# Kernel tuning notes

Measured on AMD Instinct MI355X. Metric: run time of the kernel, lower is better.

Reference implementation:

```python
import jax, jax.numpy as jnp
import numpy as np

# Representation: lvals=[0,1] -> nreps NL=2, dim DIM=1+3=4; mult=8; kqv conv out_mult=3*mult
N, K, EDGE_DIM, HID = 10000, 16, 32, 64
MULT, NL, DIM = 8, 2, 4
OUT_MULT = 3 * MULT
E = N * K
NHEADS = 4
HEAD_DIM = MULT * DIM // NHEADS  # 8


def setup_inputs() -> dict:
    key = jax.random.key(0)
    ks = jax.random.split(key, 9)
    out_flat = NL * NL * MULT * OUT_MULT  # 768
    return {
        "basis1": jax.random.normal(ks[0], (E, DIM, NL), jnp.float32),
        "basis2": jax.random.normal(ks[1], (E, NL, DIM), jnp.float32),
        "edge_feats": jax.random.normal(ks[2], (E, EDGE_DIM), jnp.float32),
        "f": jax.random.normal(ks[3], (N, MULT, DIM), jnp.float32),
        "W1": jax.random.normal(ks[4], (HID, EDGE_DIM), jnp.float32) / np.sqrt(EDGE_DIM).astype(np.float32),
        "b1": jnp.zeros((HID,), jnp.float32),
        "W2": jax.random.normal(ks[5], (out_flat, HID), jnp.float32) / np.sqrt(HID).astype(np.float32),
        "b2": jnp.zeros((out_flat,), jnp.float32),
        "neighbor_idx": jax.random.randint(ks[6], (N, K), 0, N, dtype=jnp.int32),
    }


def reference(basis1, basis2, edge_feats, f, W1, b1, W2, b2, neighbor_idx):
    src = neighbor_idx.reshape(-1)  # (E,) source node per edge
    # RadialWeight: 2-layer MLP edge_feats -> per-edge TP weights (E, NL*OUT_MULT, NL*MULT)
    h = jax.nn.relu(edge_feats @ W1.T + b1)
    rw = (h @ W2.T + b2).reshape(E, NL * OUT_MULT, NL * MULT)
    # EquivariantConvolution: gather + small batched matmuls
    f_src = f[src]  # (E, MULT, DIM)
    tmp = jnp.einsum('emd,edl->eml', f_src, basis1).reshape(E, NL * MULT, 1)
    tmp = (rw @ tmp).reshape(E, OUT_MULT, NL)
    kqv = jnp.einsum('eml,eld->emd', tmp, basis2)  # (E, 3*MULT, DIM)
    # split fused k/q/v along multiplicity (repr_h.rep2.mult = 3*mult)
    k_, q_, v_ = jnp.split(kqv.reshape(N, K, OUT_MULT, DIM), 3, axis=2)  # each (N,K,MULT,DIM)
    k_ = k_.reshape(N, K, NHEADS, HEAD_DIM)
    v_ = v_.reshape(N, K, NHEADS, HEAD_DIM)
    q_node = q_.reshape(N, K, NHEADS, HEAD_DIM).mean(axis=1)  # per-node query (N,H,hd)
    scale = HEAD_DIM ** -0.5
    scores = jnp.einsum('nhd,nkhd->nhk', q_node, k_) * scale  # (N,H,K)
    w = jax.nn.softmax(scores, axis=-1)
    out = jnp.einsum('nhk,nkhd->nhd', w, v_)  # (N,H,hd)
    return out.reshape(N, MULT, DIM)
```

## Files before the change

kernel.cpp:

```cpp
#include <hip/hip_runtime.h>
#include <hip/hip_bf16.h>
#include <math.h>

#define N_NODES 10000
#define KNBR    16
#define EDGEF   32
#define HID     64
#define MULT    8
#define NL      2
#define DIM     4
#define OUT_MULT 24
#define NHEADS  4
#define HEAD_DIM 8
#define E_TOT   (N_NODES*KNBR)

#define EPB 128
#define TPB 256
#define NODES_PB 8
#define NSLICE 33

typedef float    f32x4 __attribute__((ext_vector_type(4)));
typedef _Float16 f16x8 __attribute__((ext_vector_type(8)));

#define BF1_HALVES (4*64*8)
#define BF2_HALVES (3*NSLICE*64*8)
#define WS_HALVES  (BF1_HALVES + BF2_HALVES)

__global__ __launch_bounds__(256)
void esa_prep(const float* __restrict__ W1, const float* __restrict__ W2,
              const float* __restrict__ b2, _Float16* __restrict__ wsh)
{
    int i = blockIdx.x * 256 + threadIdx.x;
    if (i >= WS_HALVES) return;
    float v;
    if (i < BF1_HALVES) {
        int j = i & 7, lane = (i >> 3) & 63, t = i >> 9;
        int k = ((lane >> 4) << 3) + j;
        int n = (t << 4) + (lane & 15);
        v = W1[n * EDGEF + k];
    } else {
        int i2 = i - BF1_HALVES;
        int j = i2 & 7, lane = (i2 >> 3) & 63;
        int st = i2 >> 9;
        int s = st % NSLICE, t = st / NSLICE;
        int k = (s << 5) + ((lane >> 4) << 3) + j;
        int n = (t << 4) + (lane & 15);
        if (k < 1024)      v = W2[(n * 16 + (k >> 6)) * HID + (k & 63)];
        else if (k < 1040) v = b2[n * 16 + (k - 1024)];
        else               v = 0.f;
    }
    wsh[i] = (_Float16)v;
}

__global__ __launch_bounds__(TPB, 4)
void esa_main(const float* __restrict__ basis1, const float* __restrict__ basis2,
              const float* __restrict__ edge_feats, const float* __restrict__ f,
              const float* __restrict__ b1, const int* __restrict__ nbr,
              const _Float16* __restrict__ wsh, float* __restrict__ out)
{
    __shared__ __align__(16) unsigned char smem[32768];
    _Float16* hls = (_Float16*)smem;
    _Float16* tpl = (_Float16*)(smem + 18432);
    float*    t2  = (float*)smem;
    float*    b2l = (float*)(smem + 26624);

    const int tid  = threadIdx.x;
    const int eb   = blockIdx.x * EPB;
    const int lane = tid & 63;
    const int w    = tid >> 6;
    const int lo   = lane & 15, hi = lane >> 4;

    {
        int el = tid >> 1, hf = tid & 1;
        int e  = eb + el;
        int src = nbr[e];
        const float4* b1p = (const float4*)(basis1 + (size_t)e * 8);
        float4 u0 = b1p[0], u1 = b1p[1];
        float bl0[4] = {u0.x, u0.z, u1.x, u1.z};
        float bl1[4] = {u0.y, u0.w, u1.y, u1.w};
        const float4* fp = (const float4*)(f + (size_t)src * 32 + hf * 16);
        _Float16 tpv[8];
        #pragma unroll
        for (int mm = 0; mm < 4; ++mm) {
            float4 fv = fp[mm];
            float a0 = fv.x*bl0[0] + fv.y*bl0[1] + fv.z*bl0[2] + fv.w*bl0[3];
            float a1 = fv.x*bl1[0] + fv.y*bl1[1] + fv.z*bl1[2] + fv.w*bl1[3];
            tpv[mm*2+0] = (_Float16)a0;
            tpv[mm*2+1] = (_Float16)a1;
        }
        *(f16x8*)(tpl + el*16 + hf*8) = *(f16x8*)tpv;
        float4 b2v = ((const float4*)(basis2 + (size_t)e * 8))[hf];
        *((float4*)(b2l + el*12) + hf) = b2v;
    }

    {
        float b1v[4];
        #pragma unroll
        for (int t = 0; t < 4; ++t) b1v[t] = b1[t*16 + lo];
        f16x8 afr[2];
        #pragma unroll
        for (int mt = 0; mt < 2; ++mt) {
            size_t eg = (size_t)(eb + w*32 + mt*16 + lo);
            const float4* p = (const float4*)(edge_feats + eg*32 + hi*8);
            float4 x0 = p[0], x1 = p[1];
            f16x8 a;
            a[0]=(_Float16)x0.x; a[1]=(_Float16)x0.y; a[2]=(_Float16)x0.z; a[3]=(_Float16)x0.w;
            a[4]=(_Float16)x1.x; a[5]=(_Float16)x1.y; a[6]=(_Float16)x1.z; a[7]=(_Float16)x1.w;
            afr[mt] = a;
        }
        #pragma unroll
        for (int t = 0; t < 4; ++t) {
            f16x8 bfr = *(const f16x8*)(wsh + ((size_t)(t*64 + lane)) * 8);
            #pragma unroll
            for (int mt = 0; mt < 2; ++mt) {
                f32x4 acc = {0.f, 0.f, 0.f, 0.f};
                acc = __builtin_amdgcn_mfma_f32_16x16x32_f16(afr[mt], bfr, acc, 0, 0, 0);
                #pragma unroll
                for (int r = 0; r < 4; ++r) {
                    float hv = acc[r] + b1v[t];
                    hv = hv > 0.f ? hv : 0.f;
                    int el = w*32 + mt*16 + hi*4 + r;
                    hls[el*72 + t*16 + lo] = (_Float16)hv;
                }
            }
        }
    }
    __syncthreads();

    f32x4 acc[2][3];
    #pragma unroll
    for (int mt = 0; mt < 2; ++mt)
        #pragma unroll
        for (int t = 0; t < 3; ++t)
            acc[mt][t] = (f32x4){0.f, 0.f, 0.f, 0.f};

    {
        const _Float16* Bf2 = wsh + BF1_HALVES;
        const int e0 = w*32 + lo;
        const int e1 = e0 + 16;
        const _Float16* hp0 = hls + e0*72 + hi*8;
        const _Float16* hp1 = hls + e1*72 + hi*8;
        f16x8 tp0a = *(const f16x8*)(tpl + e0*16);
        f16x8 tp0b = *(const f16x8*)(tpl + e0*16 + 8);
        f16x8 tp1a = *(const f16x8*)(tpl + e1*16);
        f16x8 tp1b = *(const f16x8*)(tpl + e1*16 + 8);

        #pragma unroll 2
        for (int s = 0; s < 32; ++s) {
            const int c  = s >> 1;
            const int sh = s & 1;
            _Float16 t0 = tpl[e0*16 + c];
            _Float16 t1 = tpl[e1*16 + c];
            f16x8 ts0 = {t0,t0,t0,t0,t0,t0,t0,t0};
            f16x8 ts1 = {t1,t1,t1,t1,t1,t1,t1,t1};
            f16x8 h0 = *(const f16x8*)(hp0 + sh*32);
            f16x8 h1 = *(const f16x8*)(hp1 + sh*32);
            f16x8 a0 = h0 * ts0;
            f16x8 a1 = h1 * ts1;
            #pragma unroll
            for (int t = 0; t < 3; ++t) {
                f16x8 bfr = *(const f16x8*)(Bf2 + ((size_t)((t*NSLICE + s)*64 + lane)) * 8);
                acc[0][t] = __builtin_amdgcn_mfma_f32_16x16x32_f16(a0, bfr, acc[0][t], 0, 0, 0);
                acc[1][t] = __builtin_amdgcn_mfma_f32_16x16x32_f16(a1, bfr, acc[1][t], 0, 0, 0);
            }
        }
        {
            f16x8 z = {(_Float16)0,(_Float16)0,(_Float16)0,(_Float16)0,
                       (_Float16)0,(_Float16)0,(_Float16)0,(_Float16)0};
            f16x8 a0 = (hi == 0) ? tp0a : (hi == 1) ? tp0b : z;
            f16x8 a1 = (hi == 0) ? tp1a : (hi == 1) ? tp1b : z;
            #pragma unroll
            for (int t = 0; t < 3; ++t) {
                f16x8 bfr = *(const f16x8*)(Bf2 + ((size_t)((t*NSLICE + 32)*64 + lane)) * 8);
                acc[0][t] = __builtin_amdgcn_mfma_f32_16x16x32_f16(a0, bfr, acc[0][t], 0, 0, 0);
                acc[1][t] = __builtin_amdgcn_mfma_f32_16x16x32_f16(a1, bfr, acc[1][t], 0, 0, 0);
            }
        }
    }

    __syncthreads();
    #pragma unroll
    for (int mt = 0; mt < 2; ++mt)
        #pragma unroll
        for (int t = 0; t < 3; ++t)
            #pragma unroll
            for (int r = 0; r < 4; ++r)
                t2[(w*32 + mt*16 + hi*4 + r)*52 + t*16 + lo] = acc[mt][t][r];
    __syncthreads();

    const int kk = lane >> 2, hh = lane & 3;
    #pragma unroll
    for (int it = 0; it < 2; ++it) {
        int nl = it*4 + w;
        int node = blockIdx.x * NODES_PB + nl;
        int el = nl*16 + kk;
        const float* trow = t2 + el*52;
        float4 tk = *(const float4*)(trow + hh*4);
        float4 tq = *(const float4*)(trow + 16 + hh*4);
        float4 tv = *(const float4*)(trow + 32 + hh*4);
        float4 bl0 = *(const float4*)(b2l + el*12);
        float4 bl1 = *(const float4*)(b2l + el*12 + 4);
        float k8[8], q8[8], v8[8];
        const float* B0 = (const float*)&bl0;
        const float* B1 = (const float*)&bl1;
        #pragma unroll
        for (int d = 0; d < 4; ++d) {
            k8[d]   = tk.x*B0[d] + tk.y*B1[d];
            k8[4+d] = tk.z*B0[d] + tk.w*B1[d];
            q8[d]   = tq.x*B0[d] + tq.y*B1[d];
            q8[4+d] = tq.z*B0[d] + tq.w*B1[d];
            v8[d]   = tv.x*B0[d] + tv.y*B1[d];
            v8[4+d] = tv.z*B0[d] + tv.w*B1[d];
        }
        float qn[8];
        #pragma unroll
        for (int i = 0; i < 8; ++i) qn[i] = q8[i];
        #pragma unroll
        for (int m = 4; m <= 32; m <<= 1)
            #pragma unroll
            for (int i = 0; i < 8; ++i) qn[i] += __shfl_xor(qn[i], m);
        float s = 0.f;
        #pragma unroll
        for (int i = 0; i < 8; ++i) s += qn[i]*k8[i];
        s *= 0.0220970869120796f;

        float mx = s;
        #pragma unroll
        for (int m = 4; m <= 32; m <<= 1) mx = fmaxf(mx, __shfl_xor(mx, m));
        float ex = __expf(s - mx);
        float den = ex;
        #pragma unroll
        for (int m = 4; m <= 32; m <<= 1) den += __shfl_xor(den, m);
        float wgt = ex / den;

        float o[8];
        #pragma unroll
        for (int i = 0; i < 8; ++i) o[i] = wgt * v8[i];
        #pragma unroll
        for (int m = 4; m <= 32; m <<= 1)
            #pragma unroll
            for (int i = 0; i < 8; ++i) o[i] += __shfl_xor(o[i], m);
        if (kk == 0) {
            float4* dst = (float4*)(out + (size_t)node*32 + hh*8);
            dst[0] = make_float4(o[0], o[1], o[2], o[3]);
            dst[1] = make_float4(o[4], o[5], o[6], o[7]);
        }
    }
}

extern "C" void kernel_launch(void* const* d_in, const int* in_sizes, int n_in,
                              void* d_out, int out_size, void* d_ws, size_t ws_size,
                              hipStream_t stream) {
    const float* basis1     = (const float*)d_in[0];
    const float* basis2     = (const float*)d_in[1];
    const float* edge_feats = (const float*)d_in[2];
    const float* f          = (const float*)d_in[3];
    const float* W1         = (const float*)d_in[4];
    const float* b1         = (const float*)d_in[5];
    const float* W2         = (const float*)d_in[6];
    const float* b2         = (const float*)d_in[7];
    const int*   nbr        = (const int*)d_in[8];
    float* out = (float*)d_out;
    _Float16* wsh = (_Float16*)d_ws;

    esa_prep<<<(WS_HALVES + 255)/256, 256, 0, stream>>>(W1, W2, b2, wsh);
    esa_main<<<E_TOT/EPB, TPB, 0, stream>>>(basis1, basis2, edge_feats, f,
                                            b1, nbr, wsh, out);
}
```

Before: 128.2 us.

## Halve threads per block and give each wave four edge tiles to reuse weight fragments

The block drops to 128 threads (two waves), and each wave now handles 64 edges as four 16-row MFMA tiles instead of two. Each B-fragment load of the radial-weight matrix is reused across four tiles, halving global/L2 weight traffic per edge. The tp scalars are taken from registers rather than re-read from LDS. In exchange, accumulator register pressure doubles (launch bounds lowered to 2), per-thread prep work doubles, and fewer waves per block may reduce latency hiding.

```diff
diff --git a/kernel.cpp b/kernel.cpp
--- a/kernel.cpp
+++ b/kernel.cpp
@@ -15,7 +15,8 @@
 #define E_TOT   (N_NODES*KNBR)
 
 #define EPB 128
-#define TPB 256
+#define TPB 128
+#define NTILE 4
 #define NODES_PB 8
 #define NSLICE 33
 
@@ -52,7 +53,7 @@
     wsh[i] = (_Float16)v;
 }
 
-__global__ __launch_bounds__(TPB, 4)
+__global__ __launch_bounds__(TPB, 2)
 void esa_main(const float* __restrict__ basis1, const float* __restrict__ basis2,
               const float* __restrict__ edge_feats, const float* __restrict__ f,
               const float* __restrict__ b1, const int* __restrict__ nbr,
@@ -71,36 +72,38 @@
     const int lo   = lane & 15, hi = lane >> 4;
 
     {
-        int el = tid >> 1, hf = tid & 1;
-        int e  = eb + el;
-        int src = nbr[e];
+        const int el = tid;
+        const int e  = eb + el;
+        const int src = nbr[e];
         const float4* b1p = (const float4*)(basis1 + (size_t)e * 8);
         float4 u0 = b1p[0], u1 = b1p[1];
         float bl0[4] = {u0.x, u0.z, u1.x, u1.z};
         float bl1[4] = {u0.y, u0.w, u1.y, u1.w};
-        const float4* fp = (const float4*)(f + (size_t)src * 32 + hf * 16);
-        _Float16 tpv[8];
-        #pragma unroll
-        for (int mm = 0; mm < 4; ++mm) {
-            float4 fv = fp[mm];
+        const float4* fp = (const float4*)(f + (size_t)src * 32);
+        _Float16 tpv[16];
+        #pragma unroll
+        for (int m = 0; m < 8; ++m) {
+            float4 fv = fp[m];
             float a0 = fv.x*bl0[0] + fv.y*bl0[1] + fv.z*bl0[2] + fv.w*bl0[3];
             float a1 = fv.x*bl1[0] + fv.y*bl1[1] + fv.z*bl1[2] + fv.w*bl1[3];
-            tpv[mm*2+0] = (_Float16)a0;
-            tpv[mm*2+1] = (_Float16)a1;
-        }
-        *(f16x8*)(tpl + el*16 + hf*8) = *(f16x8*)tpv;
-        float4 b2v = ((const float4*)(basis2 + (size_t)e * 8))[hf];
-        *((float4*)(b2l + el*12) + hf) = b2v;
+            tpv[m*2+0] = (_Float16)a0;
+            tpv[m*2+1] = (_Float16)a1;
+        }
+        *(f16x8*)(tpl + el*16)     = *(f16x8*)&tpv[0];
+        *(f16x8*)(tpl + el*16 + 8) = *(f16x8*)&tpv[8];
+        const float4* b2p = (const float4*)(basis2 + (size_t)e * 8);
+        *(float4*)(b2l + el*12)     = b2p[0];
+        *(float4*)(b2l + el*12 + 4) = b2p[1];
     }
 
     {
         float b1v[4];
         #pragma unroll
         for (int t = 0; t < 4; ++t) b1v[t] = b1[t*16 + lo];
-        f16x8 afr[2];
-        #pragma unroll
-        for (int mt = 0; mt < 2; ++mt) {
-            size_t eg = (size_t)(eb + w*32 + mt*16 + lo);
+        f16x8 afr[NTILE];
+        #pragma unroll
+        for (int mt = 0; mt < NTILE; ++mt) {
+            size_t eg = (size_t)(eb + w*64 + mt*16 + lo);
             const float4* p = (const float4*)(edge_feats + eg*32 + hi*8);
             float4 x0 = p[0], x1 = p[1];
             f16x8 a;
@@ -112,14 +115,14 @@
         for (int t = 0; t < 4; ++t) {
             f16x8 bfr = *(const f16x8*)(wsh + ((size_t)(t*64 + lane)) * 8);
             #pragma unroll
-            for (int mt = 0; mt < 2; ++mt) {
+            for (int mt = 0; mt < NTILE; ++mt) {
                 f32x4 acc = {0.f, 0.f, 0.f, 0.f};
                 acc = __builtin_amdgcn_mfma_f32_16x16x32_f16(afr[mt], bfr, acc, 0, 0, 0);
                 #pragma unroll
                 for (int r = 0; r < 4; ++r) {
                     float hv = acc[r] + b1v[t];
                     hv = hv > 0.f ? hv : 0.f;
-                    int el = w*32 + mt*16 + hi*4 + r;
+                    int el = w*64 + mt*16 + hi*4 + r;
                     hls[el*72 + t*16 + lo] = (_Float16)hv;
                 }
             }
@@ -127,71 +130,75 @@
     }
     __syncthreads();
 
-    f32x4 acc[2][3];
+    f32x4 acc[NTILE][3];
     #pragma unroll
-    for (int mt = 0; mt < 2; ++mt)
+    for (int mt = 0; mt < NTILE; ++mt)
         #pragma unroll
         for (int t = 0; t < 3; ++t)
             acc[mt][t] = (f32x4){0.f, 0.f, 0.f, 0.f};
 
     {
         const _Float16* Bf2 = wsh + BF1_HALVES;
-        const int e0 = w*32 + lo;
-        const int e1 = e0 + 16;
-        const _Float16* hp0 = hls + e0*72 + hi*8;
-        const _Float16* hp1 = hls + e1*72 + hi*8;
-        f16x8 tp0a = *(const f16x8*)(tpl + e0*16);
-        f16x8 tp0b = *(const f16x8*)(tpl + e0*16 + 8);
-        f16x8 tp1a = *(const f16x8*)(tpl + e1*16);
-        f16x8 tp1b = *(const f16x8*)(tpl + e1*16 + 8);
-
-        #pragma unroll 2
+        const _Float16* hp[NTILE];
+        f16x8 tpA[NTILE], tpB[NTILE];
+        #pragma unroll
+        for (int mt = 0; mt < NTILE; ++mt) {
+            const int e_mt = w*64 + mt*16 + lo;
+            hp[mt]  = hls + e_mt*72 + hi*8;
+            tpA[mt] = *(const f16x8*)(tpl + e_mt*16);
+            tpB[mt] = *(const f16x8*)(tpl + e_mt*16 + 8);
+        }
+
+        #pragma unroll
         for (int s = 0; s < 32; ++s) {
             const int c  = s >> 1;
             const int sh = s & 1;
-            _Float16 t0 = tpl[e0*16 + c];
-            _Float16 t1 = tpl[e1*16 + c];
-            f16x8 ts0 = {t0,t0,t0,t0,t0,t0,t0,t0};
-            f16x8 ts1 = {t1,t1,t1,t1,t1,t1,t1,t1};
-            f16x8 h0 = *(const f16x8*)(hp0 + sh*32);
-            f16x8 h1 = *(const f16x8*)(hp1 + sh*32);
-            f16x8 a0 = h0 * ts0;
-            f16x8 a1 = h1 * ts1;
-            #pragma unroll
-            for (int t = 0; t < 3; ++t) {
-                f16x8 bfr = *(const f16x8*)(Bf2 + ((size_t)((t*NSLICE + s)*64 + lane)) * 8);
-                acc[0][t] = __builtin_amdgcn_mfma_f32_16x16x32_f16(a0, bfr, acc[0][t], 0, 0, 0);
-                acc[1][t] = __builtin_amdgcn_mfma_f32_16x16x32_f16(a1, bfr, acc[1][t], 0, 0, 0);
+            f16x8 bfr[3];
+            #pragma unroll
+            for (int t = 0; t < 3; ++t)
+                bfr[t] = *(const f16x8*)(Bf2 + ((size_t)((t*NSLICE + s)*64 + lane)) * 8);
+            #pragma unroll
+            for (int mt = 0; mt < NTILE; ++mt) {
+                _Float16 t0 = (c < 8) ? tpA[mt][c & 7] : tpB[mt][c & 7];
+                f16x8 ts = {t0,t0,t0,t0,t0,t0,t0,t0};
+                f16x8 h  = *(const f16x8*)(hp[mt] + sh*32);
+                f16x8 a  = h * ts;
+                #pragma unroll
+                for (int t = 0; t < 3; ++t)
+                    acc[mt][t] = __builtin_amdgcn_mfma_f32_16x16x32_f16(a, bfr[t], acc[mt][t], 0, 0, 0);
             }
         }
         {
             f16x8 z = {(_Float16)0,(_Float16)0,(_Float16)0,(_Float16)0,
                        (_Float16)0,(_Float16)0,(_Float16)0,(_Float16)0};
-            f16x8 a0 = (hi == 0) ? tp0a : (hi == 1) ? tp0b : z;
-            f16x8 a1 = (hi == 0) ? tp1a : (hi == 1) ? tp1b : z;
-            #pragma unroll
-            for (int t = 0; t < 3; ++t) {
-                f16x8 bfr = *(const f16x8*)(Bf2 + ((size_t)((t*NSLICE + 32)*64 + lane)) * 8);
-                acc[0][t] = __builtin_amdgcn_mfma_f32_16x16x32_f16(a0, bfr, acc[0][t], 0, 0, 0);
-                acc[1][t] = __builtin_amdgcn_mfma_f32_16x16x32_f16(a1, bfr, acc[1][t], 0, 0, 0);
+            f16x8 bfr[3];
+            #pragma unroll
+            for (int t = 0; t < 3; ++t)
+                bfr[t] = *(const f16x8*)(Bf2 + ((size_t)((t*NSLICE + 32)*64 + lane)) * 8);
+            #pragma unroll
+            for (int mt = 0; mt < NTILE; ++mt) {
+                f16x8 a = (hi == 0) ? tpA[mt] : (hi == 1) ? tpB[mt] : z;
+                #pragma unroll
+                for (int t = 0; t < 3; ++t)
+                    acc[mt][t] = __builtin_amdgcn_mfma_f32_16x16x32_f16(a, bfr[t], acc[mt][t], 0, 0, 0);
             }
         }
     }
 
     __syncthreads();
     #pragma unroll
-    for (int mt = 0; mt < 2; ++mt)
+    for (int mt = 0; mt < NTILE; ++mt)
         #pragma unroll
         for (int t = 0; t < 3; ++t)
             #pragma unroll
             for (int r = 0; r < 4; ++r)
-                t2[(w*32 + mt*16 + hi*4 + r)*52 + t*16 + lo] = acc[mt][t][r];
+                t2[(w*64 + mt*16 + hi*4 + r)*52 + t*16 + lo] = acc[mt][t][r];
     __syncthreads();
 
     const int kk = lane >> 2, hh = lane & 3;
     #pragma unroll
-    for (int it = 0; it < 2; ++it) {
-        int nl = it*4 + w;
+    for (int it = 0; it < 4; ++it) {
+        int nl = it*2 + w;
         int node = blockIdx.x * NODES_PB + nl;
         int el = nl*16 + kk;
         const float* trow = t2 + el*52;
```

New measurement: 124.9 us. -2.5%, faster.
